# Optimization experiments

Hardware: AMD Instinct MI355X
Metric: run time of the kernel (lower is better)

Reference implementation:

```python
import jax, jax.numpy as jnp
import numpy as np

B = 20000      # batch (edges/nodes)
DIM = 512      # irreps feature dim for x, y, and out
NNZ = 5000     # number of nonzero CG paths


def setup_inputs() -> dict:
    key = jax.random.key(0)
    k1, k2, k3, k4, k5, k6 = jax.random.split(key, 6)
    x = jax.random.normal(k1, (B, DIM), dtype=jnp.float32)
    y = jax.random.normal(k2, (B, DIM), dtype=jnp.float32)
    scale = jax.random.normal(k3, (NNZ,), dtype=jnp.float32)  # CG coefficients
    M = jnp.sort(jax.random.randint(k4, (NNZ,), 0, DIM, dtype=jnp.int32))   # scatter idx into out
    M1 = jax.random.randint(k5, (NNZ,), 0, DIM, dtype=jnp.int32)            # gather idx into x
    M2 = jax.random.randint(k6, (NNZ,), 0, DIM, dtype=jnp.int32)            # gather idx into y
    return {"x": x, "y": y, "scale": scale, "M": M, "M1": M1, "M2": M2}


def reference(x, y, scale, M, M1, M2):
    # sparse_mul: out[b, M[i]] += scale[i] * x[b, M1[i]] * y[b, M2[i]]
    prod = x[:, M1] * y[:, M2] * scale[None, :]          # [B, NNZ]
    out = jnp.zeros((x.shape[0], DIM), dtype=x.dtype)
    out = out.at[:, M].add(prod)                          # scatter-accumulate over feature axis
    return out
```

## Files before the change

kernel.cpp:

```cpp
#include <hip/hip_runtime.h>
#include <hip/hip_fp16.h>


#define BLK    256
#define RROWS  8
#define DIMC   512
#define DEPTH  8
#define SLOTS  256


__global__ void prep_kernel(const float* __restrict__ scale,
                            const int* __restrict__ M,
                            const int* __restrict__ M1,
                            const int* __restrict__ M2,
                            int2* __restrict__ pk2, int* __restrict__ starts,
                            int nnz)
{
    int i = blockIdx.x * blockDim.x + threadIdx.x;
    if (i < nnz) {
        unsigned key = (unsigned)M[i] | ((unsigned)M1[i] << 10)
                                      | ((unsigned)M2[i] << 20);
        pk2[i] = make_int2((int)key, __float_as_int(scale[i]));
    }
    if (i <= SLOTS) {
        int j = (int)((long long)i * nnz / SLOTS);
        if (j > 0 && j < nnz) {
            const int prev = M[j - 1];
            while (j < nnz && M[j] == prev) ++j;
        }
        if (j > nnz) j = nnz;
        starts[i] = j;
    }
}

__device__ __forceinline__ void fma8h(const uint4& xu, const uint4& yu,
                                      float s, float4& a0, float4& a1)
{
    const __half2 p0 = __hmul2(*(const __half2*)&xu.x, *(const __half2*)&yu.x);
    const __half2 p1 = __hmul2(*(const __half2*)&xu.y, *(const __half2*)&yu.y);
    const __half2 p2 = __hmul2(*(const __half2*)&xu.z, *(const __half2*)&yu.z);
    const __half2 p3 = __hmul2(*(const __half2*)&xu.w, *(const __half2*)&yu.w);
    a0.x = fmaf(s, __low2float(p0),  a0.x);
    a0.y = fmaf(s, __high2float(p0), a0.y);
    a0.z = fmaf(s, __low2float(p1),  a0.z);
    a0.w = fmaf(s, __high2float(p1), a0.w);
    a1.x = fmaf(s, __low2float(p2),  a1.x);
    a1.y = fmaf(s, __high2float(p2), a1.y);
    a1.z = fmaf(s, __low2float(p3),  a1.z);
    a1.w = fmaf(s, __high2float(p3), a1.w);
}

__global__ __launch_bounds__(BLK, 5) void sparse_mul_kernel(
    const float* __restrict__ x, const float* __restrict__ y,
    const int2* __restrict__ pk2, const int* __restrict__ starts,
    float* __restrict__ out, int B)
{
    __shared__ uint4  xs_u[DIMC];
    __shared__ uint4  ys_u[DIMC];
    __shared__ float4 os4[2 * DIMC];

    const int tid = threadIdx.x;
    const int b0  = blockIdx.x * RROWS;
    const bool full = (b0 + RROWS) <= B;

    #pragma unroll
    for (int f = tid; f < 2 * DIMC; f += BLK)
        os4[f] = make_float4(0.f, 0.f, 0.f, 0.f);

    for (int f = tid; f < DIMC; f += BLK) {
        const int d = f;
        float xr[RROWS], yr[RROWS];
        if (full) {
            #pragma unroll
            for (int r = 0; r < RROWS; ++r) {
                xr[r] = x[(size_t)(b0 + r) * DIMC + d];
                yr[r] = y[(size_t)(b0 + r) * DIMC + d];
            }
        } else {
            #pragma unroll
            for (int r = 0; r < RROWS; ++r) {
                const bool ok = (b0 + r) < B;
                xr[r] = ok ? x[(size_t)(b0 + r) * DIMC + d] : 0.f;
                yr[r] = ok ? y[(size_t)(b0 + r) * DIMC + d] : 0.f;
            }
        }
        uint4 xu, yu;
        {
            __half2 h0 = __floats2half2_rn(xr[0], xr[1]);
            __half2 h1 = __floats2half2_rn(xr[2], xr[3]);
            __half2 h2 = __floats2half2_rn(xr[4], xr[5]);
            __half2 h3 = __floats2half2_rn(xr[6], xr[7]);
            xu = make_uint4(*(unsigned*)&h0, *(unsigned*)&h1,
                            *(unsigned*)&h2, *(unsigned*)&h3);
            h0 = __floats2half2_rn(yr[0], yr[1]);
            h1 = __floats2half2_rn(yr[2], yr[3]);
            h2 = __floats2half2_rn(yr[4], yr[5]);
            h3 = __floats2half2_rn(yr[6], yr[7]);
            yu = make_uint4(*(unsigned*)&h0, *(unsigned*)&h1,
                            *(unsigned*)&h2, *(unsigned*)&h3);
        }
        xs_u[d] = xu;
        ys_u[d] = yu;
    }
    __syncthreads();

    const int i0 = starts[tid];
    const int ie = starts[tid + 1];

    if (i0 < ie) {
        const int last = ie - 1;

        int2 buf[DEPTH];
        #pragma unroll
        for (int j = 0; j < DEPTH; ++j) buf[j] = pk2[min(i0 + j, last)];

        float4 a0 = make_float4(0.f, 0.f, 0.f, 0.f);
        float4 a1 = make_float4(0.f, 0.f, 0.f, 0.f);

        int   mC = buf[0].x & 1023;
        int   sC = buf[0].y;
        uint4 xu = xs_u[((unsigned)buf[0].x >> 10) & 1023u];
        uint4 yu = ys_u[(unsigned)buf[0].x >> 20];
        int   cur = mC;

        for (int base = i0; base < ie; base += DEPTH) {
            int2 nxt[DEPTH];
            #pragma unroll
            for (int j = 0; j < DEPTH; ++j)
                nxt[j] = pk2[min(base + DEPTH + j, last)];

            #pragma unroll
            for (int j = 0; j < DEPTH; ++j) {
                const int2 ne = (j < DEPTH - 1) ? buf[j + 1] : nxt[0];
                const int   mN  = ne.x & 1023;
                const uint4 xuN = xs_u[((unsigned)ne.x >> 10) & 1023u];
                const uint4 yuN = ys_u[(unsigned)ne.x >> 20];

                if (mC != cur) {
                    os4[2 * cur]     = a0;
                    os4[2 * cur + 1] = a1;
                    a0 = make_float4(0.f, 0.f, 0.f, 0.f);
                    a1 = make_float4(0.f, 0.f, 0.f, 0.f);
                    cur = mC;
                }
                const float s = (base + j < ie) ? __int_as_float(sC) : 0.f;
                fma8h(xu, yu, s, a0, a1);

                mC = mN; sC = ne.y; xu = xuN; yu = yuN;
            }
            #pragma unroll
            for (int j = 0; j < DEPTH; ++j) buf[j] = nxt[j];
        }
        os4[2 * cur]     = a0;
        os4[2 * cur + 1] = a1;
    }
    __syncthreads();

    for (int f = tid; f < DIMC; f += BLK) {
        const int d = f;
        const float4 v0 = os4[2 * d];
        const float4 v1 = os4[2 * d + 1];
        if (full) {
            out[(size_t)(b0 + 0) * DIMC + d] = v0.x;
            out[(size_t)(b0 + 1) * DIMC + d] = v0.y;
            out[(size_t)(b0 + 2) * DIMC + d] = v0.z;
            out[(size_t)(b0 + 3) * DIMC + d] = v0.w;
            out[(size_t)(b0 + 4) * DIMC + d] = v1.x;
            out[(size_t)(b0 + 5) * DIMC + d] = v1.y;
            out[(size_t)(b0 + 6) * DIMC + d] = v1.z;
            out[(size_t)(b0 + 7) * DIMC + d] = v1.w;
        } else {
            const float vv[8] = {v0.x, v0.y, v0.z, v0.w, v1.x, v1.y, v1.z, v1.w};
            #pragma unroll
            for (int r = 0; r < RROWS; ++r)
                if ((b0 + r) < B) out[(size_t)(b0 + r) * DIMC + d] = vv[r];
        }
    }
}

__global__ void sparse_mul_fallback(
    const float* __restrict__ x, const float* __restrict__ y,
    const float* __restrict__ scale, const int* __restrict__ M,
    const int* __restrict__ M1, const int* __restrict__ M2,
    float* __restrict__ out, int nnz)
{
    __shared__ float orow[DIMC];
    const int b = blockIdx.x;
    for (int d = threadIdx.x; d < DIMC; d += blockDim.x) orow[d] = 0.f;
    __syncthreads();
    for (int i = threadIdx.x; i < nnz; i += blockDim.x) {
        const float v = scale[i] * x[(size_t)b * DIMC + M1[i]]
                                 * y[(size_t)b * DIMC + M2[i]];
        atomicAdd(&orow[M[i]], v);
    }
    __syncthreads();
    for (int d = threadIdx.x; d < DIMC; d += blockDim.x)
        out[(size_t)b * DIMC + d] = orow[d];
}

extern "C" void kernel_launch(void* const* d_in, const int* in_sizes, int n_in,
                              void* d_out, int out_size, void* d_ws, size_t ws_size,
                              hipStream_t stream) {
    const float* x     = (const float*)d_in[0];
    const float* y     = (const float*)d_in[1];
    const float* scale = (const float*)d_in[2];
    const int*   M     = (const int*)d_in[3];
    const int*   M1    = (const int*)d_in[4];
    const int*   M2    = (const int*)d_in[5];
    float* out = (float*)d_out;

    const int B   = in_sizes[0] / DIMC;
    const int nnz = in_sizes[2];

    const size_t need = (size_t)nnz * sizeof(int2) + (SLOTS + 1) * sizeof(int);
    if (nnz > 0 && ws_size >= need) {
        int2* pk2   = (int2*)d_ws;
        int* starts = (int*)((char*)d_ws + (size_t)nnz * sizeof(int2));
        const int pn = (nnz > SLOTS + 1) ? nnz : SLOTS + 1;
        prep_kernel<<<(pn + BLK - 1) / BLK, BLK, 0, stream>>>(
            scale, M, M1, M2, pk2, starts, nnz);
        const int grid = (B + RROWS - 1) / RROWS;
        sparse_mul_kernel<<<grid, BLK, 0, stream>>>(x, y, pk2, starts, out, B);
    } else {
        sparse_mul_fallback<<<B, BLK, 0, stream>>>(x, y, scale, M, M1, M2, out, nnz);
    }
}
```

Measured before the change: 151.6 us.

## Make sparse_mul kernel persistent and prefetch next tile during path loop

```diff
diff --git a/kernel.cpp b/kernel.cpp
--- a/kernel.cpp
+++ b/kernel.cpp
@@ -7,6 +7,7 @@
 #define DIMC   512
 #define DEPTH  8
 #define SLOTS  256
+#define GRIDB  1280
 
 
 __global__ void prep_kernel(const float* __restrict__ scale,
@@ -59,55 +60,60 @@
     __shared__ uint4  ys_u[DIMC];
     __shared__ float4 os4[2 * DIMC];
 
-    const int tid = threadIdx.x;
-    const int b0  = blockIdx.x * RROWS;
-    const bool full = (b0 + RROWS) <= B;
-
-    #pragma unroll
-    for (int f = tid; f < 2 * DIMC; f += BLK)
-        os4[f] = make_float4(0.f, 0.f, 0.f, 0.f);
-
-    for (int f = tid; f < DIMC; f += BLK) {
-        const int d = f;
-        float xr[RROWS], yr[RROWS];
-        if (full) {
-            #pragma unroll
-            for (int r = 0; r < RROWS; ++r) {
-                xr[r] = x[(size_t)(b0 + r) * DIMC + d];
-                yr[r] = y[(size_t)(b0 + r) * DIMC + d];
-            }
-        } else {
-            #pragma unroll
-            for (int r = 0; r < RROWS; ++r) {
-                const bool ok = (b0 + r) < B;
-                xr[r] = ok ? x[(size_t)(b0 + r) * DIMC + d] : 0.f;
-                yr[r] = ok ? y[(size_t)(b0 + r) * DIMC + d] : 0.f;
-            }
-        }
-        uint4 xu, yu;
-        {
-            __half2 h0 = __floats2half2_rn(xr[0], xr[1]);
-            __half2 h1 = __floats2half2_rn(xr[2], xr[3]);
-            __half2 h2 = __floats2half2_rn(xr[4], xr[5]);
-            __half2 h3 = __floats2half2_rn(xr[6], xr[7]);
-            xu = make_uint4(*(unsigned*)&h0, *(unsigned*)&h1,
-                            *(unsigned*)&h2, *(unsigned*)&h3);
-            h0 = __floats2half2_rn(yr[0], yr[1]);
-            h1 = __floats2half2_rn(yr[2], yr[3]);
-            h2 = __floats2half2_rn(yr[4], yr[5]);
-            h3 = __floats2half2_rn(yr[6], yr[7]);
-            yu = make_uint4(*(unsigned*)&h0, *(unsigned*)&h1,
-                            *(unsigned*)&h2, *(unsigned*)&h3);
-        }
-        xs_u[d] = xu;
-        ys_u[d] = yu;
-    }
-    __syncthreads();
+    const int tid    = threadIdx.x;
+    const int ntiles = (B + RROWS - 1) / RROWS;
 
     const int i0 = starts[tid];
     const int ie = starts[tid + 1];
 
-    if (i0 < ie) {
+    float xr[2 * RROWS], yr[2 * RROWS];
+
+    auto LOADT = [&](int tile) {
+        const int b0   = tile * RROWS;
+        const bool full = (b0 + RROWS) <= B;
+        #pragma unroll
+        for (int u = 0; u < 2; ++u) {
+            const int d = tid + u * BLK;
+            if (full) {
+                #pragma unroll
+                for (int r = 0; r < RROWS; ++r) {
+                    xr[u * RROWS + r] = x[(size_t)(b0 + r) * DIMC + d];
+                    yr[u * RROWS + r] = y[(size_t)(b0 + r) * DIMC + d];
+                }
+            } else {
+                #pragma unroll
+                for (int r = 0; r < RROWS; ++r) {
+                    const bool ok = (b0 + r) < B;
+                    xr[u * RROWS + r] = ok ? x[(size_t)(b0 + r) * DIMC + d] : 0.f;
+                    yr[u * RROWS + r] = ok ? y[(size_t)(b0 + r) * DIMC + d] : 0.f;
+                }
+            }
+        }
+    };
+
+    auto CVTSTORE = [&]() {
+        #pragma unroll
+        for (int u = 0; u < 2; ++u) {
+            const int d = tid + u * BLK;
+            const float* xp = &xr[u * RROWS];
+            const float* yp = &yr[u * RROWS];
+            __half2 h0 = __floats2half2_rn(xp[0], xp[1]);
+            __half2 h1 = __floats2half2_rn(xp[2], xp[3]);
+            __half2 h2 = __floats2half2_rn(xp[4], xp[5]);
+            __half2 h3 = __floats2half2_rn(xp[6], xp[7]);
+            xs_u[d] = make_uint4(*(unsigned*)&h0, *(unsigned*)&h1,
+                                 *(unsigned*)&h2, *(unsigned*)&h3);
+            h0 = __floats2half2_rn(yp[0], yp[1]);
+            h1 = __floats2half2_rn(yp[2], yp[3]);
+            h2 = __floats2half2_rn(yp[4], yp[5]);
+            h3 = __floats2half2_rn(yp[6], yp[7]);
+            ys_u[d] = make_uint4(*(unsigned*)&h0, *(unsigned*)&h1,
+                                 *(unsigned*)&h2, *(unsigned*)&h3);
+        }
+    };
+
+    auto PATHLOOP = [&]() {
+        if (i0 >= ie) return;
         const int last = ie - 1;
 
         int2 buf[DEPTH];
@@ -124,14 +130,9 @@
         int   cur = mC;
 
         for (int base = i0; base < ie; base += DEPTH) {
-            int2 nxt[DEPTH];
-            #pragma unroll
-            for (int j = 0; j < DEPTH; ++j)
-                nxt[j] = pk2[min(base + DEPTH + j, last)];
-
             #pragma unroll
             for (int j = 0; j < DEPTH; ++j) {
-                const int2 ne = (j < DEPTH - 1) ? buf[j + 1] : nxt[0];
+                const int2 ne = buf[(j + 1) & (DEPTH - 1)];
                 const int   mN  = ne.x & 1023;
                 const uint4 xuN = xs_u[((unsigned)ne.x >> 10) & 1023u];
                 const uint4 yuN = ys_u[(unsigned)ne.x >> 20];
@@ -146,35 +147,61 @@
                 const float s = (base + j < ie) ? __int_as_float(sC) : 0.f;
                 fma8h(xu, yu, s, a0, a1);
 
+                buf[j] = pk2[min(base + DEPTH + j, last)];
+
                 mC = mN; sC = ne.y; xu = xuN; yu = yuN;
             }
-            #pragma unroll
-            for (int j = 0; j < DEPTH; ++j) buf[j] = nxt[j];
         }
         os4[2 * cur]     = a0;
         os4[2 * cur + 1] = a1;
-    }
+    };
+
+    auto WRITEBACK = [&](int tile) {
+        const int b0   = tile * RROWS;
+        const bool full = (b0 + RROWS) <= B;
+        #pragma unroll
+        for (int u = 0; u < 2; ++u) {
+            const int d = tid + u * BLK;
+            const float4 v0 = os4[2 * d];
+            const float4 v1 = os4[2 * d + 1];
+            os4[2 * d]     = make_float4(0.f, 0.f, 0.f, 0.f);
+            os4[2 * d + 1] = make_float4(0.f, 0.f, 0.f, 0.f);
+            if (full) {
+                out[(size_t)(b0 + 0) * DIMC + d] = v0.x;
+                out[(size_t)(b0 + 1) * DIMC + d] = v0.y;
+                out[(size_t)(b0 + 2) * DIMC + d] = v0.z;
+                out[(size_t)(b0 + 3) * DIMC + d] = v0.w;
+                out[(size_t)(b0 + 4) * DIMC + d] = v1.x;
+                out[(size_t)(b0 + 5) * DIMC + d] = v1.y;
+                out[(size_t)(b0 + 6) * DIMC + d] = v1.z;
+                out[(size_t)(b0 + 7) * DIMC + d] = v1.w;
+            } else {
+                const float vv[8] = {v0.x, v0.y, v0.z, v0.w,
+                                     v1.x, v1.y, v1.z, v1.w};
+                #pragma unroll
+                for (int r = 0; r < RROWS; ++r)
+                    if ((b0 + r) < B) out[(size_t)(b0 + r) * DIMC + d] = vv[r];
+            }
+        }
+    };
+
+    int tile = blockIdx.x;
+    if (tile >= ntiles) return;
+
+    for (int f = tid; f < 2 * DIMC; f += BLK)
+        os4[f] = make_float4(0.f, 0.f, 0.f, 0.f);
+    LOADT(tile);
+    CVTSTORE();
     __syncthreads();
 
-    for (int f = tid; f < DIMC; f += BLK) {
-        const int d = f;
-        const float4 v0 = os4[2 * d];
-        const float4 v1 = os4[2 * d + 1];
-        if (full) {
-            out[(size_t)(b0 + 0) * DIMC + d] = v0.x;
-            out[(size_t)(b0 + 1) * DIMC + d] = v0.y;
-            out[(size_t)(b0 + 2) * DIMC + d] = v0.z;
-            out[(size_t)(b0 + 3) * DIMC + d] = v0.w;
-            out[(size_t)(b0 + 4) * DIMC + d] = v1.x;
-            out[(size_t)(b0 + 5) * DIMC + d] = v1.y;
-            out[(size_t)(b0 + 6) * DIMC + d] = v1.z;
-            out[(size_t)(b0 + 7) * DIMC + d] = v1.w;
-        } else {
-            const float vv[8] = {v0.x, v0.y, v0.z, v0.w, v1.x, v1.y, v1.z, v1.w};
-            #pragma unroll
-            for (int r = 0; r < RROWS; ++r)
-                if ((b0 + r) < B) out[(size_t)(b0 + r) * DIMC + d] = vv[r];
-        }
+    for (; tile < ntiles; tile += GRIDB) {
+        const int tn = tile + GRIDB;
+        if (tn < ntiles) LOADT(tn);
+        PATHLOOP();
+        __syncthreads();
+        WRITEBACK(tile);
+        if (tn < ntiles) CVTSTORE();
+        __syncthreads();
     }
 }
 
@@ -219,7 +246,8 @@
         const int pn = (nnz > SLOTS + 1) ? nnz : SLOTS + 1;
         prep_kernel<<<(pn + BLK - 1) / BLK, BLK, 0, stream>>>(
             scale, M, M1, M2, pk2, starts, nnz);
-        const int grid = (B + RROWS - 1) / RROWS;
+        const int ntiles = (B + RROWS - 1) / RROWS;
+        const int grid   = ntiles < GRIDB ? ntiles : GRIDB;
         sparse_mul_kernel<<<grid, BLK, 0, stream>>>(x, y, pk2, starts, out, B);
     } else {
         sparse_mul_fallback<<<B, BLK, 0, stream>>>(x, y, scale, M, M1, M2, out, nnz);
```

After: 197.4 us. 30.2% more time.

## Persistent warp-specialized kernel with double-buffered staging of x/y tiles

Applied to the files above, without the earlier changes.

```diff
diff --git a/kernel.cpp b/kernel.cpp
--- a/kernel.cpp
+++ b/kernel.cpp
@@ -2,11 +2,12 @@
 #include <hip/hip_fp16.h>
 
 
-#define BLK    256
+#define BLK    512
+#define CONS   384
 #define RROWS  8
 #define DIMC   512
 #define DEPTH  8
-#define SLOTS  256
+#define NBLK   768
 
 
 __global__ void prep_kernel(const float* __restrict__ scale,
@@ -22,8 +23,8 @@
                                       | ((unsigned)M2[i] << 20);
         pk2[i] = make_int2((int)key, __float_as_int(scale[i]));
     }
-    if (i <= SLOTS) {
-        int j = (int)((long long)i * nnz / SLOTS);
+    if (i <= CONS) {
+        int j = (int)((long long)i * nnz / CONS);
         if (j > 0 && j < nnz) {
             const int prev = M[j - 1];
             while (j < nnz && M[j] == prev) ++j;
@@ -50,65 +51,60 @@
     a1.w = fmaf(s, __high2float(p3), a1.w);
 }
 
-__global__ __launch_bounds__(BLK, 5) void sparse_mul_kernel(
+__global__ __launch_bounds__(BLK, 6) void sparse_mul_kernel(
     const float* __restrict__ x, const float* __restrict__ y,
     const int2* __restrict__ pk2, const int* __restrict__ starts,
     float* __restrict__ out, int B)
 {
-    __shared__ uint4  xs_u[DIMC];
-    __shared__ uint4  ys_u[DIMC];
+    __shared__ uint4  xs_u[2][DIMC];
+    __shared__ uint4  ys_u[2][DIMC];
     __shared__ float4 os4[2 * DIMC];
 
-    const int tid = threadIdx.x;
-    const int b0  = blockIdx.x * RROWS;
-    const bool full = (b0 + RROWS) <= B;
-
-    #pragma unroll
-    for (int f = tid; f < 2 * DIMC; f += BLK)
-        os4[f] = make_float4(0.f, 0.f, 0.f, 0.f);
-
-    for (int f = tid; f < DIMC; f += BLK) {
-        const int d = f;
-        float xr[RROWS], yr[RROWS];
-        if (full) {
-            #pragma unroll
-            for (int r = 0; r < RROWS; ++r) {
-                xr[r] = x[(size_t)(b0 + r) * DIMC + d];
-                yr[r] = y[(size_t)(b0 + r) * DIMC + d];
+    const int tid    = threadIdx.x;
+    const int ntiles = (B + RROWS - 1) / RROWS;
+
+    const int i0 = (tid < CONS) ? starts[tid]     : 0;
+    const int ie = (tid < CONS) ? starts[tid + 1] : 0;
+
+    auto STAGE = [&](int bufi, int tile, int lane0, int nl) {
+        const int b0   = tile * RROWS;
+        const bool full = (b0 + RROWS) <= B;
+        for (int d = tid - lane0; d < DIMC; d += nl) {
+            float xr[RROWS], yr[RROWS];
+            if (full) {
+                #pragma unroll
+                for (int r = 0; r < RROWS; ++r) {
+                    xr[r] = x[(size_t)(b0 + r) * DIMC + d];
+                    yr[r] = y[(size_t)(b0 + r) * DIMC + d];
+                }
+            } else {
+                #pragma unroll
+                for (int r = 0; r < RROWS; ++r) {
+                    const bool ok = (b0 + r) < B;
+                    xr[r] = ok ? x[(size_t)(b0 + r) * DIMC + d] : 0.f;
+                    yr[r] = ok ? y[(size_t)(b0 + r) * DIMC + d] : 0.f;
+                }
             }
-        } else {
-            #pragma unroll
-            for (int r = 0; r < RROWS; ++r) {
-                const bool ok = (b0 + r) < B;
-                xr[r] = ok ? x[(size_t)(b0 + r) * DIMC + d] : 0.f;
-                yr[r] = ok ? y[(size_t)(b0 + r) * DIMC + d] : 0.f;
-            }
-        }
-        uint4 xu, yu;
-        {
             __half2 h0 = __floats2half2_rn(xr[0], xr[1]);
             __half2 h1 = __floats2half2_rn(xr[2], xr[3]);
             __half2 h2 = __floats2half2_rn(xr[4], xr[5]);
             __half2 h3 = __floats2half2_rn(xr[6], xr[7]);
-            xu = make_uint4(*(unsigned*)&h0, *(unsigned*)&h1,
-                            *(unsigned*)&h2, *(unsigned*)&h3);
+            xs_u[bufi][d] = make_uint4(*(unsigned*)&h0, *(unsigned*)&h1,
+                                       *(unsigned*)&h2, *(unsigned*)&h3);
             h0 = __floats2half2_rn(yr[0], yr[1]);
             h1 = __floats2half2_rn(yr[2], yr[3]);
             h2 = __floats2half2_rn(yr[4], yr[5]);
             h3 = __floats2half2_rn(yr[6], yr[7]);
-            yu = make_uint4(*(unsigned*)&h0, *(unsigned*)&h1,
-                            *(unsigned*)&h2, *(unsigned*)&h3);
-        }
-        xs_u[d] = xu;
-        ys_u[d] = yu;
-    }
-    __syncthreads();
-
-    const int i0 = starts[tid];
-    const int ie = starts[tid + 1];
-
-    if (i0 < ie) {
+            ys_u[bufi][d] = make_uint4(*(unsigned*)&h0, *(unsigned*)&h1,
+                                       *(unsigned*)&h2, *(unsigned*)&h3);
+        }
+    };
+
+    auto PATHLOOP = [&](int bufi) {
+        if (i0 >= ie) return;
         const int last = ie - 1;
+        const uint4* __restrict__ xs = xs_u[bufi];
+        const uint4* __restrict__ ys = ys_u[bufi];
 
         int2 buf[DEPTH];
         #pragma unroll
@@ -119,22 +115,17 @@
 
         int   mC = buf[0].x & 1023;
         int   sC = buf[0].y;
-        uint4 xu = xs_u[((unsigned)buf[0].x >> 10) & 1023u];
-        uint4 yu = ys_u[(unsigned)buf[0].x >> 20];
+        uint4 xu = xs[((unsigned)buf[0].x >> 10) & 1023u];
+        uint4 yu = ys[(unsigned)buf[0].x >> 20];
         int   cur = mC;
 
         for (int base = i0; base < ie; base += DEPTH) {
-            int2 nxt[DEPTH];
-            #pragma unroll
-            for (int j = 0; j < DEPTH; ++j)
-                nxt[j] = pk2[min(base + DEPTH + j, last)];
-
             #pragma unroll
             for (int j = 0; j < DEPTH; ++j) {
-                const int2 ne = (j < DEPTH - 1) ? buf[j + 1] : nxt[0];
+                const int2 ne = buf[(j + 1) & (DEPTH - 1)];
                 const int   mN  = ne.x & 1023;
-                const uint4 xuN = xs_u[((unsigned)ne.x >> 10) & 1023u];
-                const uint4 yuN = ys_u[(unsigned)ne.x >> 20];
+                const uint4 xuN = xs[((unsigned)ne.x >> 10) & 1023u];
+                const uint4 yuN = ys[(unsigned)ne.x >> 20];
 
                 if (mC != cur) {
                     os4[2 * cur]     = a0;
@@ -146,20 +137,23 @@
                 const float s = (base + j < ie) ? __int_as_float(sC) : 0.f;
                 fma8h(xu, yu, s, a0, a1);
 
+                buf[j] = pk2[min(base + DEPTH + j, last)];
+
                 mC = mN; sC = ne.y; xu = xuN; yu = yuN;
             }
-            #pragma unroll
-            for (int j = 0; j < DEPTH; ++j) buf[j] = nxt[j];
         }
         os4[2 * cur]     = a0;
         os4[2 * cur + 1] = a1;
-    }
-    __syncthreads();
-
-    for (int f = tid; f < DIMC; f += BLK) {
-        const int d = f;
+    };
+
+    auto WRITEBACK = [&](int tile) {
+        const int b0   = tile * RROWS;
+        const bool full = (b0 + RROWS) <= B;
+        const int d = tid;
         const float4 v0 = os4[2 * d];
         const float4 v1 = os4[2 * d + 1];
+        os4[2 * d]     = make_float4(0.f, 0.f, 0.f, 0.f);
+        os4[2 * d + 1] = make_float4(0.f, 0.f, 0.f, 0.f);
         if (full) {
             out[(size_t)(b0 + 0) * DIMC + d] = v0.x;
             out[(size_t)(b0 + 1) * DIMC + d] = v0.y;
@@ -170,11 +164,37 @@
             out[(size_t)(b0 + 6) * DIMC + d] = v1.z;
             out[(size_t)(b0 + 7) * DIMC + d] = v1.w;
         } else {
-            const float vv[8] = {v0.x, v0.y, v0.z, v0.w, v1.x, v1.y, v1.z, v1.w};
-            #pragma unroll
-            for (int r = 0; r < RROWS; ++r)
-                if ((b0 + r) < B) out[(size_t)(b0 + r) * DIMC + d] = vv[r];
-        }
+            if ((b0 + 0) < B) out[(size_t)(b0 + 0) * DIMC + d] = v0.x;
+            if ((b0 + 1) < B) out[(size_t)(b0 + 1) * DIMC + d] = v0.y;
+            if ((b0 + 2) < B) out[(size_t)(b0 + 2) * DIMC + d] = v0.z;
+            if ((b0 + 3) < B) out[(size_t)(b0 + 3) * DIMC + d] = v0.w;
+            if ((b0 + 4) < B) out[(size_t)(b0 + 4) * DIMC + d] = v1.x;
+            if ((b0 + 5) < B) out[(size_t)(b0 + 5) * DIMC + d] = v1.y;
+            if ((b0 + 6) < B) out[(size_t)(b0 + 6) * DIMC + d] = v1.z;
+            if ((b0 + 7) < B) out[(size_t)(b0 + 7) * DIMC + d] = v1.w;
+        }
+    };
+
+    int tile = blockIdx.x;
+    if (tile >= ntiles) return;
+
+    os4[tid]       = make_float4(0.f, 0.f, 0.f, 0.f);
+    os4[tid + BLK] = make_float4(0.f, 0.f, 0.f, 0.f);
+    STAGE(0, tile, 0, BLK);
+    __syncthreads();
+
+    int cur = 0;
+    for (; tile < ntiles; tile += NBLK) {
+        const int tn = tile + NBLK;
+        if (tid < CONS) {
+            PATHLOOP(cur);
+        } else if (tn < ntiles) {
+            STAGE(cur ^ 1, tn, CONS, BLK - CONS);
+        }
+        __syncthreads();
+        WRITEBACK(tile);
+        cur ^= 1;
+        __syncthreads();
     }
 }
 
@@ -212,16 +232,18 @@
     const int B   = in_sizes[0] / DIMC;
     const int nnz = in_sizes[2];
 
-    const size_t need = (size_t)nnz * sizeof(int2) + (SLOTS + 1) * sizeof(int);
+    const size_t need = (size_t)nnz * sizeof(int2) + (CONS + 1) * sizeof(int);
     if (nnz > 0 && ws_size >= need) {
         int2* pk2   = (int2*)d_ws;
         int* starts = (int*)((char*)d_ws + (size_t)nnz * sizeof(int2));
-        const int pn = (nnz > SLOTS + 1) ? nnz : SLOTS + 1;
-        prep_kernel<<<(pn + BLK - 1) / BLK, BLK, 0, stream>>>(
+        const int pn = (nnz > CONS + 1) ? nnz : CONS + 1;
+        const int pblk = 256;
+        prep_kernel<<<(pn + pblk - 1) / pblk, pblk, 0, stream>>>(
             scale, M, M1, M2, pk2, starts, nnz);
-        const int grid = (B + RROWS - 1) / RROWS;
+        const int ntiles = (B + RROWS - 1) / RROWS;
+        const int grid   = ntiles < NBLK ? ntiles : NBLK;
         sparse_mul_kernel<<<grid, BLK, 0, stream>>>(x, y, pk2, starts, out, B);
     } else {
-        sparse_mul_fallback<<<B, BLK, 0, stream>>>(x, y, scale, M, M1, M2, out, nnz);
-    }
-}
+        sparse_mul_fallback<<<B, 256, 0, stream>>>(x, y, scale, M, M1, M2, out, nnz);
+    }
+}
```

Result: slower. 206.6 us (+36.3%).

## Split NNZ evenly per thread and merge boundary segments with shared atomics

Applied to the files above, without the earlier changes.

```diff
diff --git a/kernel.cpp b/kernel.cpp
--- a/kernel.cpp
+++ b/kernel.cpp
@@ -6,30 +6,19 @@
 #define RROWS  8
 #define DIMC   512
 #define DEPTH  8
-#define SLOTS  256
 
 
 __global__ void prep_kernel(const float* __restrict__ scale,
                             const int* __restrict__ M,
                             const int* __restrict__ M1,
                             const int* __restrict__ M2,
-                            int2* __restrict__ pk2, int* __restrict__ starts,
-                            int nnz)
+                            int2* __restrict__ pk2, int nnz)
 {
     int i = blockIdx.x * blockDim.x + threadIdx.x;
     if (i < nnz) {
         unsigned key = (unsigned)M[i] | ((unsigned)M1[i] << 10)
                                       | ((unsigned)M2[i] << 20);
         pk2[i] = make_int2((int)key, __float_as_int(scale[i]));
-    }
-    if (i <= SLOTS) {
-        int j = (int)((long long)i * nnz / SLOTS);
-        if (j > 0 && j < nnz) {
-            const int prev = M[j - 1];
-            while (j < nnz && M[j] == prev) ++j;
-        }
-        if (j > nnz) j = nnz;
-        starts[i] = j;
     }
 }
 
@@ -52,8 +41,8 @@
 
 __global__ __launch_bounds__(BLK, 5) void sparse_mul_kernel(
     const float* __restrict__ x, const float* __restrict__ y,
-    const int2* __restrict__ pk2, const int* __restrict__ starts,
-    float* __restrict__ out, int B)
+    const int2* __restrict__ pk2, float* __restrict__ out,
+    int B, int nnz)
 {
     __shared__ uint4  xs_u[DIMC];
     __shared__ uint4  ys_u[DIMC];
@@ -63,7 +52,6 @@
     const int b0  = blockIdx.x * RROWS;
     const bool full = (b0 + RROWS) <= B;
 
-    #pragma unroll
     for (int f = tid; f < 2 * DIMC; f += BLK)
         os4[f] = make_float4(0.f, 0.f, 0.f, 0.f);
 
@@ -104,8 +92,8 @@
     }
     __syncthreads();
 
-    const int i0 = starts[tid];
-    const int ie = starts[tid + 1];
+    const int i0 = (int)((long long)tid       * nnz / BLK);
+    const int ie = (int)((long long)(tid + 1) * nnz / BLK);
 
     if (i0 < ie) {
         const int last = ie - 1;
@@ -122,23 +110,28 @@
         uint4 xu = xs_u[((unsigned)buf[0].x >> 10) & 1023u];
         uint4 yu = ys_u[(unsigned)buf[0].x >> 20];
         int   cur = mC;
+        bool  firstFlush = true;
 
         for (int base = i0; base < ie; base += DEPTH) {
-            int2 nxt[DEPTH];
-            #pragma unroll
-            for (int j = 0; j < DEPTH; ++j)
-                nxt[j] = pk2[min(base + DEPTH + j, last)];
-
             #pragma unroll
             for (int j = 0; j < DEPTH; ++j) {
-                const int2 ne = (j < DEPTH - 1) ? buf[j + 1] : nxt[0];
+                const int2 ne = buf[(j + 1) & (DEPTH - 1)];
                 const int   mN  = ne.x & 1023;
                 const uint4 xuN = xs_u[((unsigned)ne.x >> 10) & 1023u];
                 const uint4 yuN = ys_u[(unsigned)ne.x >> 20];
 
                 if (mC != cur) {
-                    os4[2 * cur]     = a0;
-                    os4[2 * cur + 1] = a1;
+                    if (firstFlush) {
+                        float* o = (float*)&os4[2 * cur];
+                        atomicAdd(o + 0, a0.x); atomicAdd(o + 1, a0.y);
+                        atomicAdd(o + 2, a0.z); atomicAdd(o + 3, a0.w);
+                        atomicAdd(o + 4, a1.x); atomicAdd(o + 5, a1.y);
+                        atomicAdd(o + 6, a1.z); atomicAdd(o + 7, a1.w);
+                        firstFlush = false;
+                    } else {
+                        os4[2 * cur]     = a0;
+                        os4[2 * cur + 1] = a1;
+                    }
                     a0 = make_float4(0.f, 0.f, 0.f, 0.f);
                     a1 = make_float4(0.f, 0.f, 0.f, 0.f);
                     cur = mC;
@@ -146,13 +139,18 @@
                 const float s = (base + j < ie) ? __int_as_float(sC) : 0.f;
                 fma8h(xu, yu, s, a0, a1);
 
+                buf[j] = pk2[min(base + DEPTH + j, last)];
+
                 mC = mN; sC = ne.y; xu = xuN; yu = yuN;
             }
-            #pragma unroll
-            for (int j = 0; j < DEPTH; ++j) buf[j] = nxt[j];
-        }
-        os4[2 * cur]     = a0;
-        os4[2 * cur + 1] = a1;
+        }
+        {
+            float* o = (float*)&os4[2 * cur];
+            atomicAdd(o + 0, a0.x); atomicAdd(o + 1, a0.y);
+            atomicAdd(o + 2, a0.z); atomicAdd(o + 3, a0.w);
+            atomicAdd(o + 4, a1.x); atomicAdd(o + 5, a1.y);
+            atomicAdd(o + 6, a1.z); atomicAdd(o + 7, a1.w);
+        }
     }
     __syncthreads();
 
@@ -212,15 +210,13 @@
     const int B   = in_sizes[0] / DIMC;
     const int nnz = in_sizes[2];
 
-    const size_t need = (size_t)nnz * sizeof(int2) + (SLOTS + 1) * sizeof(int);
+    const size_t need = (size_t)nnz * sizeof(int2);
     if (nnz > 0 && ws_size >= need) {
-        int2* pk2   = (int2*)d_ws;
-        int* starts = (int*)((char*)d_ws + (size_t)nnz * sizeof(int2));
-        const int pn = (nnz > SLOTS + 1) ? nnz : SLOTS + 1;
-        prep_kernel<<<(pn + BLK - 1) / BLK, BLK, 0, stream>>>(
-            scale, M, M1, M2, pk2, starts, nnz);
+        int2* pk2 = (int2*)d_ws;
+        prep_kernel<<<(nnz + BLK - 1) / BLK, BLK, 0, stream>>>(
+            scale, M, M1, M2, pk2, nnz);
         const int grid = (B + RROWS - 1) / RROWS;
-        sparse_mul_kernel<<<grid, BLK, 0, stream>>>(x, y, pk2, starts, out, B);
+        sparse_mul_kernel<<<grid, BLK, 0, stream>>>(x, y, pk2, out, B, nnz);
     } else {
         sparse_mul_fallback<<<B, BLK, 0, stream>>>(x, y, scale, M, M1, M2, out, nnz);
     }
```

Result: slower. 187.1 us (+23.4%).
